# Optimization experiments

Hardware: AMD Instinct MI355X
Metric: run time of the kernel (lower is better)

The kernel has to match this reference:

```python
import jax, jax.numpy as jnp
import numpy as np

N = 256      # Lx * Ly sites
NH = 64      # GRU hidden units
K = 2        # local Hilbert space dim


def setup_inputs() -> dict:
    key = jax.random.key(0)
    k1, k2, k3, k4, k5 = jax.random.split(key, 5)
    # scale weights down to keep sigmoid/tanh/softmax in a sane range
    return {
        "numsamples": 8192,
        "Wi": jax.random.normal(k1, (K, 3 * NH), jnp.float32) * 0.1,
        "Wh": jax.random.normal(k2, (NH, 3 * NH), jnp.float32) * 0.1,
        "b": jax.random.normal(k3, (2, 3 * NH), jnp.float32) * 0.1,
        "Wd": jax.random.normal(k4, (NH, K), jnp.float32) * 0.1,
        "bd": jax.random.normal(k5, (K,), jnp.float32) * 0.1,
    }


def _gru_cell(x, h, Wi, Wh, b):
    # keras GRU with reset_after=True (default)
    mx = x @ Wi + b[0]           # [B, 3*NH]
    mh = h @ Wh + b[1]           # [B, 3*NH]
    xz, xr, xh = jnp.split(mx, 3, axis=-1)
    rz, rr, rh = jnp.split(mh, 3, axis=-1)
    z = jax.nn.sigmoid(xz + rz)
    r = jax.nn.sigmoid(xr + rr)
    hh = jnp.tanh(xh + r * rh)
    return z * h + (1.0 - z) * hh


def reference(numsamples, Wi, Wh, b, Wd, bd):
    B = numsamples
    keys = jax.random.split(jax.random.key(1234), N)

    def step(carry, key):
        h, inp = carry                         # h: [B,NH], inp: [B,K] one-hot
        h = _gru_cell(inp, h, Wi, Wh, b)
        logits = h @ Wd + bd                   # [B,K]
        logp = jax.nn.log_softmax(logits)      # log of dense-softmax output
        s = jax.random.categorical(key, logits)  # [B] int
        chosen = jnp.take_along_axis(logp, s[:, None], axis=1)[:, 0]
        inp_new = jax.nn.one_hot(s, K, dtype=jnp.float32)
        return (h, inp_new), (s, chosen)

    h0 = jnp.zeros((B, NH), jnp.float32)
    inp0 = jnp.zeros((B, K), jnp.float32)
    _, (samples, chosen_logp) = jax.lax.scan(step, (h0, inp0), keys)
    samples = samples.T.astype(jnp.float32)           # [B, N]
    log_probs = 0.5 * jnp.sum(chosen_logp, axis=0)    # [B]
    return samples, log_probs
```

## Files before the change

kernel.cpp:

```cpp
#include <hip/hip_runtime.h>
#include <stdint.h>

#define NSITES 256
#define NHID   64
#define BATCH  8192

typedef float v4f __attribute__((ext_vector_type(4)));
typedef short v8s __attribute__((ext_vector_type(8)));

__device__ __forceinline__ uint32_t rotl32(uint32_t v, int d) {
  return (v << d) | (v >> (32 - d));
}

__device__ __forceinline__ void tf2x32(uint32_t k0, uint32_t k1,
                                       uint32_t x0, uint32_t x1,
                                       uint32_t& o0, uint32_t& o1) {
  uint32_t ks2 = k0 ^ k1 ^ 0x1BD11BDAu;
  x0 += k0; x1 += k1;
#define TFR4(a,b,c,d) \
  x0 += x1; x1 = rotl32(x1,a); x1 ^= x0; \
  x0 += x1; x1 = rotl32(x1,b); x1 ^= x0; \
  x0 += x1; x1 = rotl32(x1,c); x1 ^= x0; \
  x0 += x1; x1 = rotl32(x1,d); x1 ^= x0;
  TFR4(13,15,26,6)   x0 += k1;  x1 += ks2 + 1u;
  TFR4(17,29,16,24)  x0 += ks2; x1 += k0  + 2u;
  TFR4(13,15,26,6)   x0 += k0;  x1 += k1  + 3u;
  TFR4(17,29,16,24)  x0 += k1;  x1 += ks2 + 4u;
  TFR4(13,15,26,6)   x0 += ks2; x1 += k0  + 5u;
#undef TFR4
  o0 = x0; o1 = x1;
}

__device__ __forceinline__ float gumb_from_bits(uint32_t bits) {
  float f = __uint_as_float((bits >> 9) | 0x3f800000u) - 1.0f;
  float u = (f == 0.0f) ? 1.17549435e-38f : f;
  return -logf(-logf(u));
}

__device__ __forceinline__ uint32_t rbits32(uint32_t k0, uint32_t k1, uint32_t e) {
  uint32_t a, b;
  tf2x32(k0, k1, 0u, e, a, b);
  return a ^ b;
}

__global__ void gumbel_precompute(float2* __restrict__ g) {
  int idx = blockIdx.x * blockDim.x + threadIdx.x;
  if (idx >= NSITES * BATCH) return;
  int t = idx >> 13;
  int b = idx & (BATCH - 1);
  uint32_t kt0, kt1;
  tf2x32(0u, 1234u, 0u, (uint32_t)t, kt0, kt1);
  uint32_t r0 = rbits32(kt0, kt1, (uint32_t)(2 * b));
  uint32_t r1 = rbits32(kt0, kt1, (uint32_t)(2 * b + 1));
  g[idx] = make_float2(gumb_from_bits(r0), gumb_from_bits(r1));
}

__global__ void split_awt(const float* __restrict__ Wh, const float* __restrict__ Wd,
                          ushort* __restrict__ w0, ushort* __restrict__ w1,
                          ushort* __restrict__ w2) {
  int idx = blockIdx.x * 256 + threadIdx.x;
  if (idx >= 208 * 64) return;
  int col = idx >> 6;
  int j   = idx & 63;
  float w;
  if (col < 192)      w = Wh[j * 192 + col];
  else if (col < 194) w = Wd[j * 2 + (col - 192)];
  else                w = 0.0f;
  uint32_t u0 = __float_as_uint(w) & 0xffff0000u;
  float f0 = __uint_as_float(u0);
  float r1 = w - f0;
  uint32_t u1 = __float_as_uint(r1) & 0xffff0000u;
  float f1 = __uint_as_float(u1);
  float r2 = r1 - f1;
  uint32_t u2 = __float_as_uint(r2) & 0xffff0000u;
  w0[idx] = (ushort)(u0 >> 16);
  w1[idx] = (ushort)(u1 >> 16);
  w2[idx] = (ushort)(u2 >> 16);
}

__device__ __forceinline__ float sigmoid_xla(float x) {
  return 0.5f + 0.5f * tanhf(0.5f * x);
}

#define MF(A_, B_, C_) __builtin_amdgcn_mfma_f32_16x16x32_bf16((A_), (B_), (C_), 0, 0, 0)
#define F4(v_, r_) (((const float*)&(v_))[r_])

__global__ __launch_bounds__(256, 2)
void rnn_mfma7(const float* __restrict__ Wi, const float* __restrict__ bb,
               const float* __restrict__ bd,
               const ushort* __restrict__ w0p, const ushort* __restrict__ w1p,
               const ushort* __restrict__ w2p, const float2* __restrict__ g,
               float* __restrict__ out_s, float* __restrict__ out_lp) {
  __shared__ __align__(16) ushort bsp[2][3072];
  __shared__ __align__(16) float c0zr[128];
  __shared__ __align__(16) float bh0a[64], bh1a[64];
  __shared__ __align__(16) float cw0[192], cw1[192];

  const int tid = threadIdx.x;
  const int l = tid & 63, s = l & 15, hi = l >> 4;
  const int w = tid >> 6;
  const int base = blockIdx.x * 16;

  if (tid < 64) {
    c0zr[tid] = bb[tid] + bb[192 + tid];
    c0zr[tid + 64] = bb[tid + 64] + bb[256 + tid];
    bh0a[tid] = bb[128 + tid];
    bh1a[tid] = bb[320 + tid];
    cw0[tid] = Wi[tid]; cw0[tid + 64] = Wi[tid + 64]; cw0[tid + 128] = Wi[tid + 128];
    cw1[tid] = Wi[192 + tid]; cw1[tid + 64] = Wi[256 + tid]; cw1[tid + 128] = Wi[320 + tid];
  }
  for (int k = tid; k < 1536; k += 256) ((uint*)bsp[0])[k] = 0u;
  __syncthreads();

  v8s A0[3][2], A1[3][2], A2[3][2];
#pragma unroll
  for (int i3 = 0; i3 < 3; ++i3) {
    const int tile = w + 4 * i3;
#pragma unroll
    for (int kc = 0; kc < 2; ++kc) {
      const int off = (16 * tile + s) * 64 + 32 * kc + 8 * hi;
      A0[i3][kc] = *reinterpret_cast<const v8s*>(w0p + off);
      A1[i3][kc] = *reinterpret_cast<const v8s*>(w1p + off);
      A2[i3][kc] = *reinterpret_cast<const v8s*>(w2p + off);
    }
  }
  v8s L0[2], L1[2], L2[2];
#pragma unroll
  for (int kc = 0; kc < 2; ++kc) {
    const int off = (192 + s) * 64 + 32 * kc + 8 * hi;
    L0[kc] = *reinterpret_cast<const v8s*>(w0p + off);
    L1[kc] = *reinterpret_cast<const v8s*>(w1p + off);
    L2[kc] = *reinterpret_cast<const v8s*>(w2p + off);
  }

  const float bd0 = bd[0], bd1 = bd[1];
  const int u0i = 16 * w + 4 * hi;
  const float4 czv  = *reinterpret_cast<const float4*>(&c0zr[u0i]);
  const float4 crv  = *reinterpret_cast<const float4*>(&c0zr[64 + u0i]);
  const float4 bh0v = *reinterpret_cast<const float4*>(&bh0a[u0i]);
  const float4 bh1v = *reinterpret_cast<const float4*>(&bh1a[u0i]);
  const float4 wz0  = *reinterpret_cast<const float4*>(&cw0[u0i]);
  const float4 wz1  = *reinterpret_cast<const float4*>(&cw1[u0i]);
  const float4 wr0  = *reinterpret_cast<const float4*>(&cw0[64 + u0i]);
  const float4 wr1  = *reinterpret_cast<const float4*>(&cw1[64 + u0i]);
  const float4 wh0  = *reinterpret_cast<const float4*>(&cw0[128 + u0i]);
  const float4 wh1  = *reinterpret_cast<const float4*>(&cw1[128 + u0i]);

  const int kcw = w >> 1;
  const int hgw = (2 * w + (hi >> 1)) & 3;
  const int i0  = (hi & 1) * 4;

  float hreg[4] = {0.0f, 0.0f, 0.0f, 0.0f};
  float lp = 0.0f;
  float2 gcur = make_float2(0.0f, 0.0f), gnext = make_float2(0.0f, 0.0f);
  int p = 0;

  for (int t = 0; t <= NSITES; ++t) {
    if (t < NSITES && hi == 0) gnext = g[t * BATCH + base + s];

    const ushort* rb = bsp[p] + hi * 128 + s * 8;
    v8s B0[2], B1[2], B2[2];
#pragma unroll
    for (int kc = 0; kc < 2; ++kc) {
      B0[kc] = *reinterpret_cast<const v8s*>(rb + kc * 512);
      B1[kc] = *reinterpret_cast<const v8s*>(rb + 1024 + kc * 512);
      B2[kc] = *reinterpret_cast<const v8s*>(rb + 2048 + kc * 512);
    }

    v4f al = {0.0f, 0.0f, 0.0f, 0.0f};
#pragma unroll
    for (int kc = 0; kc < 2; ++kc) al = MF(L1[kc], B1[kc], al);
#pragma unroll
    for (int kc = 0; kc < 2; ++kc) al = MF(L2[kc], B0[kc], al);
#pragma unroll
    for (int kc = 0; kc < 2; ++kc) al = MF(L0[kc], B2[kc], al);
#pragma unroll
    for (int kc = 0; kc < 2; ++kc) al = MF(L1[kc], B0[kc], al);
#pragma unroll
    for (int kc = 0; kc < 2; ++kc) al = MF(L0[kc], B1[kc], al);
#pragma unroll
    for (int kc = 0; kc < 2; ++kc) al = MF(L0[kc], B0[kc], al);

    v4f acc[3];
    if (t < NSITES) {
#pragma unroll
      for (int i3 = 0; i3 < 3; ++i3) {
        v4f a = {0.0f, 0.0f, 0.0f, 0.0f};
#pragma unroll
        for (int kc = 0; kc < 2; ++kc) a = MF(A2[i3][kc], B0[kc], a);
#pragma unroll
        for (int kc = 0; kc < 2; ++kc) a = MF(A0[i3][kc], B2[kc], a);
#pragma unroll
        for (int kc = 0; kc < 2; ++kc) a = MF(A1[i3][kc], B1[kc], a);
#pragma unroll
        for (int kc = 0; kc < 2; ++kc) a = MF(A1[i3][kc], B0[kc], a);
#pragma unroll
        for (int kc = 0; kc < 2; ++kc) a = MF(A0[i3][kc], B1[kc], a);
#pragma unroll
        for (int kc = 0; kc < 2; ++kc) a = MF(A0[i3][kc], B0[kc], a);
        acc[i3] = a;
      }
    }

    int scd = 0;
    if (t > 0) {
      const float l0 = al[0] + bd0, l1 = al[1] + bd1;
      const float mmax = fmaxf(l0, l1);
      const float sh0 = l0 - mmax, sh1 = l1 - mmax;
      const float lse = logf(expf(sh0) + expf(sh1));
      scd = ((l1 + gcur.y) > (l0 + gcur.x)) ? 1 : 0;
      lp += (scd ? sh1 : sh0) - lse;
      if (tid < 16) out_s[(size_t)(base + s) * NSITES + (t - 1)] = (float)scd;
    }

    if (t < NSITES) {
      const int scb = __shfl(scd, s, 64);

      float selz[4], selr[4], selh[4];
      if (t == 0) {
#pragma unroll
        for (int r = 0; r < 4; ++r) { selz[r] = 0.0f; selr[r] = 0.0f; selh[r] = 0.0f; }
      } else {
#pragma unroll
        for (int r = 0; r < 4; ++r) {
          selz[r] = scb ? F4(wz1, r) : F4(wz0, r);
          selr[r] = scb ? F4(wr1, r) : F4(wr0, r);
          selh[r] = scb ? F4(wh1, r) : F4(wh0, r);
        }
      }

      uint sp0[4], sp1[4], sp2[4];
#pragma unroll
      for (int r = 0; r < 4; ++r) {
        const float zin = acc[0][r] + F4(czv, r) + selz[r];
        const float rin = acc[1][r] + F4(crv, r) + selr[r];
        const float rhv = acc[2][r] + F4(bh1v, r);
        const float xhv = F4(bh0v, r) + selh[r];
        const float zg = sigmoid_xla(zin);
        const float rg = sigmoid_xla(rin);
        const float hg = tanhf(xhv + rg * rhv);
        const float hn = zg * hreg[r] + (1.0f - zg) * hg;
        hreg[r] = hn;
        const uint u0 = __float_as_uint(hn) & 0xffff0000u;
        const float f0 = __uint_as_float(u0);
        const float r1f = hn - f0;
        const uint u1 = __float_as_uint(r1f) & 0xffff0000u;
        const float f1 = __uint_as_float(u1);
        const float r2f = r1f - f1;
        const uint u2 = __float_as_uint(r2f) & 0xffff0000u;
        sp0[r] = u0 >> 16; sp1[r] = u1 >> 16; sp2[r] = u2 >> 16;
      }
      ushort* wb = bsp[p ^ 1] + kcw * 512 + hgw * 128 + s * 8 + i0;
      {
        uint2 q;
        q.x = sp0[0] | (sp0[1] << 16); q.y = sp0[2] | (sp0[3] << 16);
        *reinterpret_cast<uint2*>(wb) = q;
        q.x = sp1[0] | (sp1[1] << 16); q.y = sp1[2] | (sp1[3] << 16);
        *reinterpret_cast<uint2*>(wb + 1024) = q;
        q.x = sp2[0] | (sp2[1] << 16); q.y = sp2[2] | (sp2[3] << 16);
        *reinterpret_cast<uint2*>(wb + 2048) = q;
      }
    }

    __syncthreads();
    p ^= 1;
    gcur = gnext;
  }

  if (tid < 16) out_lp[base + s] = 0.5f * lp;
}

__global__ __launch_bounds__(64)
void rnn_plain(const float* __restrict__ Wi, const float* __restrict__ Wh,
               const float* __restrict__ bb, const float* __restrict__ Wd,
               const float* __restrict__ bd,
               float* __restrict__ out_s, float* __restrict__ out_lp) {
  const int lane = threadIdx.x;
  const int b = blockIdx.x;

  float wz[NHID], wr[NHID], wh[NHID];
#pragma unroll
  for (int j = 0; j < NHID; ++j) {
    wz[j] = Wh[j * 192 + lane];
    wr[j] = Wh[j * 192 + 64 + lane];
    wh[j] = Wh[j * 192 + 128 + lane];
  }
  const float b1z = bb[192 + lane];
  const float b1r = bb[192 + 64 + lane];
  const float b1h = bb[192 + 128 + lane];
  const float m0z = bb[lane], m0r = bb[64 + lane], m0h = bb[128 + lane];
  const float m1z = Wi[lane] + m0z, m1r = Wi[64 + lane] + m0r, m1h = Wi[128 + lane] + m0h;
  const float m2z = Wi[192 + lane] + m0z, m2r = Wi[192 + 64 + lane] + m0r,
              m2h = Wi[192 + 128 + lane] + m0h;
  const float wd0 = Wd[lane * 2 + 0], wd1 = Wd[lane * 2 + 1];
  const float bd0 = bd[0], bd1 = bd[1];

  float h = 0.0f, lpsum = 0.0f;
  float xz = m0z, xr = m0r, xh = m0h;

  for (int t = 0; t < NSITES; ++t) {
    uint32_t kt0, kt1;
    tf2x32(0u, 1234u, 0u, (uint32_t)t, kt0, kt1);
    const float g0 = gumb_from_bits(rbits32(kt0, kt1, (uint32_t)(2 * b)));
    const float g1 = gumb_from_bits(rbits32(kt0, kt1, (uint32_t)(2 * b + 1)));

    float az = 0.0f, ar = 0.0f, ah = 0.0f;
#pragma unroll
    for (int j = 0; j < NHID; ++j) {
      const float hj = __int_as_float(__builtin_amdgcn_readlane(__float_as_int(h), j));
      az = fmaf(hj, wz[j], az);
      ar = fmaf(hj, wr[j], ar);
      ah = fmaf(hj, wh[j], ah);
    }
    const float rz = az + b1z, rr = ar + b1r, rh = ah + b1h;
    const float zg = sigmoid_xla(xz + rz);
    const float rg = sigmoid_xla(xr + rr);
    const float hg = tanhf(xh + rg * rh);
    h = zg * h + (1.0f - zg) * hg;

    float p0 = h * wd0, p1 = h * wd1;
#pragma unroll
    for (int off = 32; off > 0; off >>= 1) {
      p0 += __shfl_xor(p0, off, 64);
      p1 += __shfl_xor(p1, off, 64);
    }
    const float l0 = p0 + bd0, l1 = p1 + bd1;
    const float mmax = fmaxf(l0, l1);
    const float sh0 = l0 - mmax, sh1 = l1 - mmax;
    const float lse = logf(expf(sh0) + expf(sh1));
    const int si = ((l1 + g1) > (l0 + g0)) ? 1 : 0;
    lpsum += (si ? sh1 : sh0) - lse;
    if (lane == 0) out_s[(size_t)b * NSITES + t] = (float)si;
    xz = si ? m2z : m1z;
    xr = si ? m2r : m1r;
    xh = si ? m2h : m1h;
  }

  if (lane == 0) out_lp[b] = 0.5f * lpsum;
}

extern "C" void kernel_launch(void* const* d_in, const int* in_sizes, int n_in,
                              void* d_out, int out_size, void* d_ws, size_t ws_size,
                              hipStream_t stream) {
  const float* Wi = (const float*)d_in[1];
  const float* Wh = (const float*)d_in[2];
  const float* bb = (const float*)d_in[3];
  const float* Wd = (const float*)d_in[4];
  const float* bd = (const float*)d_in[5];

  float* out    = (float*)d_out;
  float* out_s  = out;
  float* out_lp = out + (size_t)BATCH * NSITES;

  const size_t gbytes = (size_t)NSITES * BATCH * sizeof(float2);
  const size_t wb = (size_t)208 * 64 * sizeof(ushort);

  if (ws_size >= gbytes + 3 * wb) {
    float2* g  = (float2*)d_ws;
    ushort* w0 = (ushort*)((char*)d_ws + gbytes);
    ushort* w1 = w0 + 208 * 64;
    ushort* w2 = w1 + 208 * 64;
    gumbel_precompute<<<(NSITES * BATCH) / 256, 256, 0, stream>>>(g);
    split_awt<<<(208 * 64 + 255) / 256, 256, 0, stream>>>(Wh, Wd, w0, w1, w2);
    rnn_mfma7<<<BATCH / 16, 256, 0, stream>>>(Wi, bb, bd, w0, w1, w2, g, out_s, out_lp);
  } else {
    rnn_plain<<<BATCH, 64, 0, stream>>>(Wi, Wh, bb, Wd, bd, out_s, out_lp);
  }
}
```

Before: 421.4 us.

## Fuse Gumbel noise generation into RNN kernel via shared memory

```diff
diff --git a/kernel.cpp b/kernel.cpp
--- a/kernel.cpp
+++ b/kernel.cpp
@@ -43,18 +43,6 @@
   return a ^ b;
 }
 
-__global__ void gumbel_precompute(float2* __restrict__ g) {
-  int idx = blockIdx.x * blockDim.x + threadIdx.x;
-  if (idx >= NSITES * BATCH) return;
-  int t = idx >> 13;
-  int b = idx & (BATCH - 1);
-  uint32_t kt0, kt1;
-  tf2x32(0u, 1234u, 0u, (uint32_t)t, kt0, kt1);
-  uint32_t r0 = rbits32(kt0, kt1, (uint32_t)(2 * b));
-  uint32_t r1 = rbits32(kt0, kt1, (uint32_t)(2 * b + 1));
-  g[idx] = make_float2(gumb_from_bits(r0), gumb_from_bits(r1));
-}
-
 __global__ void split_awt(const float* __restrict__ Wh, const float* __restrict__ Wd,
                           ushort* __restrict__ w0, ushort* __restrict__ w1,
                           ushort* __restrict__ w2) {
@@ -63,9 +51,12 @@
   int col = idx >> 6;
   int j   = idx & 63;
   float w;
-  if (col < 192)      w = Wh[j * 192 + col];
-  else if (col < 194) w = Wd[j * 2 + (col - 192)];
-  else                w = 0.0f;
+  if (col < 192) {
+    w = Wh[j * 192 + col];
+  } else {
+    const int which = (col - 192) & 3;
+    w = (which == 0) ? Wd[j * 2] : (which == 1) ? Wd[j * 2 + 1] : 0.0f;
+  }
   uint32_t u0 = __float_as_uint(w) & 0xffff0000u;
   float f0 = __uint_as_float(u0);
   float r1 = w - f0;
@@ -86,12 +77,13 @@
 #define F4(v_, r_) (((const float*)&(v_))[r_])
 
 __global__ __launch_bounds__(256, 2)
-void rnn_mfma7(const float* __restrict__ Wi, const float* __restrict__ bb,
+void rnn_mfma9(const float* __restrict__ Wi, const float* __restrict__ bb,
                const float* __restrict__ bd,
                const ushort* __restrict__ w0p, const ushort* __restrict__ w1p,
-               const ushort* __restrict__ w2p, const float2* __restrict__ g,
+               const ushort* __restrict__ w2p,
                float* __restrict__ out_s, float* __restrict__ out_lp) {
   __shared__ __align__(16) ushort bsp[2][3072];
+  __shared__ __align__(16) float2 gl[NSITES * 16];
   __shared__ __align__(16) float c0zr[128];
   __shared__ __align__(16) float bh0a[64], bh1a[64];
   __shared__ __align__(16) float cw0[192], cw1[192];
@@ -110,6 +102,17 @@
     cw1[tid] = Wi[192 + tid]; cw1[tid + 64] = Wi[256 + tid]; cw1[tid + 128] = Wi[320 + tid];
   }
   for (int k = tid; k < 1536; k += 256) ((uint*)bsp[0])[k] = 0u;
+
+  {
+    uint32_t kt0, kt1;
+    tf2x32(0u, 1234u, 0u, (uint32_t)tid, kt0, kt1);
+    for (int k = 0; k < 16; ++k) {
+      const int bidx = base + k;
+      const float g0 = gumb_from_bits(rbits32(kt0, kt1, (uint32_t)(2 * bidx)));
+      const float g1 = gumb_from_bits(rbits32(kt0, kt1, (uint32_t)(2 * bidx + 1)));
+      gl[tid * 16 + k] = make_float2(g0, g1);
+    }
+  }
   __syncthreads();
 
   v8s A0[3][2], A1[3][2], A2[3][2];
@@ -152,12 +155,9 @@
 
   float hreg[4] = {0.0f, 0.0f, 0.0f, 0.0f};
   float lp = 0.0f;
-  float2 gcur = make_float2(0.0f, 0.0f), gnext = make_float2(0.0f, 0.0f);
   int p = 0;
 
   for (int t = 0; t <= NSITES; ++t) {
-    if (t < NSITES && hi == 0) gnext = g[t * BATCH + base + s];
-
     const ushort* rb = bsp[p] + hi * 128 + s * 8;
     v8s B0[2], B1[2], B2[2];
 #pragma unroll
@@ -204,18 +204,17 @@
 
     int scd = 0;
     if (t > 0) {
+      const float2 gc = gl[(t - 1) * 16 + s];
       const float l0 = al[0] + bd0, l1 = al[1] + bd1;
       const float mmax = fmaxf(l0, l1);
       const float sh0 = l0 - mmax, sh1 = l1 - mmax;
       const float lse = logf(expf(sh0) + expf(sh1));
-      scd = ((l1 + gcur.y) > (l0 + gcur.x)) ? 1 : 0;
+      scd = ((l1 + gc.y) > (l0 + gc.x)) ? 1 : 0;
       lp += (scd ? sh1 : sh0) - lse;
       if (tid < 16) out_s[(size_t)(base + s) * NSITES + (t - 1)] = (float)scd;
     }
 
     if (t < NSITES) {
-      const int scb = __shfl(scd, s, 64);
-
       float selz[4], selr[4], selh[4];
       if (t == 0) {
 #pragma unroll
@@ -223,9 +222,9 @@
       } else {
 #pragma unroll
         for (int r = 0; r < 4; ++r) {
-          selz[r] = scb ? F4(wz1, r) : F4(wz0, r);
-          selr[r] = scb ? F4(wr1, r) : F4(wr0, r);
-          selh[r] = scb ? F4(wh1, r) : F4(wh0, r);
+          selz[r] = scd ? F4(wz1, r) : F4(wz0, r);
+          selr[r] = scd ? F4(wr1, r) : F4(wr0, r);
+          selh[r] = scd ? F4(wh1, r) : F4(wh0, r);
         }
       }
 
@@ -264,7 +263,6 @@
 
     __syncthreads();
     p ^= 1;
-    gcur = gnext;
   }
 
   if (tid < 16) out_lp[base + s] = 0.5f * lp;
@@ -352,17 +350,14 @@
   float* out_s  = out;
   float* out_lp = out + (size_t)BATCH * NSITES;
 
-  const size_t gbytes = (size_t)NSITES * BATCH * sizeof(float2);
   const size_t wb = (size_t)208 * 64 * sizeof(ushort);
 
-  if (ws_size >= gbytes + 3 * wb) {
-    float2* g  = (float2*)d_ws;
-    ushort* w0 = (ushort*)((char*)d_ws + gbytes);
+  if (ws_size >= 3 * wb) {
+    ushort* w0 = (ushort*)d_ws;
     ushort* w1 = w0 + 208 * 64;
     ushort* w2 = w1 + 208 * 64;
-    gumbel_precompute<<<(NSITES * BATCH) / 256, 256, 0, stream>>>(g);
     split_awt<<<(208 * 64 + 255) / 256, 256, 0, stream>>>(Wh, Wd, w0, w1, w2);
-    rnn_mfma7<<<BATCH / 16, 256, 0, stream>>>(Wi, bb, bd, w0, w1, w2, g, out_s, out_lp);
+    rnn_mfma9<<<BATCH / 16, 256, 0, stream>>>(Wi, bb, bd, w0, w1, w2, out_s, out_lp);
   } else {
     rnn_plain<<<BATCH, 64, 0, stream>>>(Wi, Wh, bb, Wd, bd, out_s, out_lp);
   }
```

Result: faster. 402.9 us (-4.4%).
